# Kernel optimization log

Hardware: AMD Instinct MI355X
Metric: run time of the kernel (lower is better)

## Reference

```python
import jax, jax.numpy as jnp
import numpy as np

ALPHA = 100.0  # self.softmax_alpha


def _interp_nearest(x, size):
    # torch F.interpolate mode='nearest': src_idx = floor(dst_idx * H_in / H_out)
    H, W = x.shape[-2], x.shape[-1]
    h, w = size
    ri = (jnp.arange(h) * H) // h
    ci = (jnp.arange(w) * W) // w
    return x[:, :, ri, :][:, :, :, ci]


def _interp_bilinear_ac(x, size):
    # torch F.interpolate mode='bilinear', align_corners=True
    H, W = x.shape[-2], x.shape[-1]
    h, w = size

    def coords(n_out, n_in):
        if n_out == 1:
            return jnp.zeros((1,), jnp.float32)
        return jnp.arange(n_out, dtype=jnp.float32) * ((n_in - 1) / (n_out - 1))

    ry, rx = coords(h, H), coords(w, W)
    y0 = jnp.floor(ry).astype(jnp.int32)
    x0 = jnp.floor(rx).astype(jnp.int32)
    y1 = jnp.clip(y0 + 1, 0, H - 1)
    x1 = jnp.clip(x0 + 1, 0, W - 1)
    wy = (ry - y0.astype(jnp.float32))[None, None, :, None]
    wx = (rx - x0.astype(jnp.float32))[None, None, None, :]
    rows = x[:, :, y0, :] * (1.0 - wy) + x[:, :, y1, :] * wy  # (n,c,h,W)
    return rows[:, :, :, x0] * (1.0 - wx) + rows[:, :, :, x1] * wx  # (n,c,h,w)


def _warp(unalign_fb, fa, fa_parse, fb, fb_parse, alpha):
    n, c, h, w = fa.shape
    c2 = unalign_fb.shape[1]
    hw = h * w
    # center and channel-normalize features per spatial location
    fa = fa - jnp.mean(fa, axis=(2, 3), keepdims=True)
    fb = fb - jnp.mean(fb, axis=(2, 3), keepdims=True)
    fa = fa.reshape(n, c, hw)
    fb = fb.reshape(n, c, hw)
    fa = fa / jnp.linalg.norm(fa, axis=1, keepdims=True)
    fb = fb / jnp.linalg.norm(fb, axis=1, keepdims=True)
    ufb = unalign_fb.reshape(n, c2, hw)
    mask_a = (fa_parse.reshape(n, -1, hw)[:, 1:, :] != 0).astype(fa.dtype)  # (n,K,hw)
    mask_b = (fb_parse.reshape(n, -1, hw)[:, 1:, :] != 0).astype(fb.dtype)
    local_fa = fa[:, None, :, :] * mask_a[:, :, None, :]  # (n,K,c,hw)
    local_fb = fb[:, None, :, :] * mask_b[:, :, None, :]  # (n,K,c,hw)
    # energy[n,k,q,p] = sum_c local_fb[n,k,c,q] * local_fa[n,k,c,p]
    energy = jnp.einsum('nkcq,nkcp->nkqp', local_fb, local_fa) * alpha
    corr = jax.nn.softmax(energy, axis=2)  # softmax over fb locations q
    warped = jnp.einsum('ncq,nkqp->nkcp', ufb, corr)  # (n,K,c2,hw)
    combined = (warped * mask_a[:, :, None, :]).sum(axis=1)  # (n,c2,hw)
    norm = jnp.maximum(mask_a.sum(axis=1, keepdims=True), 1.0)  # (n,1,hw)
    aligned = combined / norm
    return aligned.reshape(n, c2, h, w)


def setup_inputs() -> dict:
    key = jax.random.key(0)
    k1, k2, k3, k4, k5 = jax.random.split(key, 5)
    return {
        'unalign_fb': jax.random.normal(k1, (1, 64, 256, 256), jnp.float32),
        'fa': jax.random.normal(k2, (1, 256, 64, 64), jnp.float32),
        'fa_parse': jax.random.randint(k3, (1, 4, 256, 256), 0, 2).astype(jnp.int32),
        'fb': jax.random.normal(k4, (1, 256, 64, 64), jnp.float32),
        'fb_parse': jax.random.randint(k5, (1, 4, 256, 256), 0, 2).astype(jnp.int32),
    }


def reference(unalign_fb, fa, fa_parse, fb, fb_parse):
    raw_hw = unalign_fb.shape[-2:]
    feat_hw = fa.shape[-2:]
    fa_p = _interp_nearest(fa_parse, feat_hw)
    fb_p = _interp_nearest(fb_parse, feat_hw)
    ufb = _interp_bilinear_ac(unalign_fb, fb.shape[-2:])
    aligned = _warp(ufb, fa, fa_p, fb, fb_p, ALPHA)
    return _interp_bilinear_ac(aligned, raw_hw)
```

## Files before the change

### kernel.cpp

```cpp
#include <hip/hip_runtime.h>
#include <math.h>

#define HW 4096
#define CC 256
#define C2 64
#define E50f 1.928749848e-22f

typedef unsigned short USH;
typedef __attribute__((ext_vector_type(8))) _Float16 f16x8;
typedef __attribute__((ext_vector_type(8))) short bf8;
typedef __attribute__((ext_vector_type(4))) float f32x4;

__device__ __forceinline__ USH f2bf(float x) {
    unsigned u = __float_as_uint(x);
    u += 0x7fff + ((u >> 16) & 1);
    return (USH)(u >> 16);
}
__device__ __forceinline__ USH f2h(float x) {
    _Float16 h = (_Float16)x;
    return *(USH*)&h;
}

__device__ __forceinline__ void gl2lds16(const USH* g, USH* l) {
    __builtin_amdgcn_global_load_lds(
        (const __attribute__((address_space(1))) void*)g,
        (__attribute__((address_space(3))) void*)l, 16, 0, 0);
}

__global__ void k_prep1(const float* __restrict__ fa, const float* __restrict__ fb,
                        float* __restrict__ mu,
                        const float* __restrict__ ufb_src, const int* __restrict__ fb_parse,
                        USH* __restrict__ vtT, float* __restrict__ bgp) {
    __shared__ float4 sred[256];
    int t = threadIdx.x;
    if (blockIdx.x < 512) {
        int b = blockIdx.x;
        const float* src = (b < CC) ? (fa + b * HW) : (fb + (b - CC) * HW);
        float s = 0.f;
        for (int q = t; q < HW; q += 256) s += src[q];
        sred[t].x = s;
        __syncthreads();
        for (int st = 128; st > 0; st >>= 1) {
            if (t < st) sred[t].x += sred[t + st].x;
            __syncthreads();
        }
        if (t == 0) mu[b] = sred[0].x * (1.0f / HW);
        return;
    }
    int bid = blockIdx.x - 512;
    int pblk = bid & 15, c = bid >> 4;
    int p = pblk * 256 + t;
    int j = p >> 6, i = p & 63;
    int off = (4 * j) * 256 + 4 * i;
    float m0 = (fb_parse[1 * 65536 + off] != 0) ? 1.f : 0.f;
    float m1 = (fb_parse[2 * 65536 + off] != 0) ? 1.f : 0.f;
    float m2 = (fb_parse[3 * 65536 + off] != 0) ? 1.f : 0.f;
    float ry = j * (255.0f / 63.0f);
    int y0 = (int)ry; y0 = min(y0, 255); int y1 = min(y0 + 1, 255);
    float wy = ry - (float)y0;
    float rx = i * (255.0f / 63.0f);
    int x0 = (int)rx; x0 = min(x0, 255); int x1 = min(x0 + 1, 255);
    float wx = rx - (float)x0;
    const float* sc = ufb_src + c * 65536;
    float r0 = sc[y0 * 256 + x0] * (1.f - wx) + sc[y0 * 256 + x1] * wx;
    float r1 = sc[y1 * 256 + x0] * (1.f - wx) + sc[y1 * 256 + x1] * wx;
    float v = r0 * (1.f - wy) + r1 * wy;
    size_t cbase = (size_t)(p >> 5) * 8192 + (p & 31);
    vtT[cbase + (0 * 65 + c) * 32] = f2bf(v * m0);
    vtT[cbase + (1 * 65 + c) * 32] = f2bf(v * m1);
    vtT[cbase + (2 * 65 + c) * 32] = f2bf(v * m2);
    if (c == 0) {
        vtT[cbase + 64 * 32]  = f2bf(m0);
        vtT[cbase + 129 * 32] = f2bf(m1);
        vtT[cbase + 194 * 32] = f2bf(m2);
        for (int m = 195; m < 256; ++m) vtT[cbase + m * 32] = 0;
    }
    sred[t] = make_float4(v, v * m0, v * m1, v * m2);
    __syncthreads();
    for (int st = 128; st > 0; st >>= 1) {
        if (t < st) {
            float4 o = sred[t + st];
            sred[t].x += o.x; sred[t].y += o.y; sred[t].z += o.z; sred[t].w += o.w;
        }
        __syncthreads();
    }
    if (t == 0) {
        float4 r = sred[0];
        bgp[pblk * 320 + 256 + c]     = r.x;
        bgp[pblk * 320 + 0 * 65 + c]  = r.y;
        bgp[pblk * 320 + 1 * 65 + c]  = r.z;
        bgp[pblk * 320 + 2 * 65 + c]  = r.w;
    }
    __syncthreads();
    if (c == 0) {
        sred[t] = make_float4(m0, m1, m2, 0.f);
        __syncthreads();
        for (int st = 128; st > 0; st >>= 1) {
            if (t < st) {
                float4 o = sred[t + st];
                sred[t].x += o.x; sred[t].y += o.y; sred[t].z += o.z;
            }
            __syncthreads();
        }
        if (t == 0) {
            float4 r = sred[0];
            bgp[pblk * 320 + 64]  = r.x;
            bgp[pblk * 320 + 129] = r.y;
            bgp[pblk * 320 + 194] = r.z;
        }
    }
}

__global__ __launch_bounds__(256) void k_normT(
    const float* __restrict__ fa, const float* __restrict__ fb,
    const float* __restrict__ mu_,
    USH* __restrict__ faT, USH* __restrict__ fbT) {
    __shared__ float tile[256][33];
    __shared__ float red[8][32];
    __shared__ float rv[32];
    int which = blockIdx.z;
    const float* src = which ? fb : fa;
    USH* dst = which ? fbT : faT;
    const float* mu = mu_ + which * CC;
    int p0 = blockIdx.x * 32;
    int t = threadIdx.x;
    int pi = t & 31, g = t >> 5;
    for (int it = 0; it < 32; ++it) {
        int c = it * 8 + g;
        tile[c][pi] = src[(size_t)c * HW + p0 + pi];
    }
    __syncthreads();
    float ss = 0.f;
#pragma unroll
    for (int jc = 0; jc < 32; ++jc) {
        float v = tile[g * 32 + jc][pi] - mu[g * 32 + jc];
        ss += v * v;
    }
    red[g][pi] = ss;
    __syncthreads();
    if (g == 0) {
        float s2 = 0.f;
#pragma unroll
        for (int gg = 0; gg < 8; ++gg) s2 += red[gg][pi];
        rv[pi] = rsqrtf(s2);
    }
    __syncthreads();
    float rinv = rv[pi];
    size_t base = (size_t)g * 131072 + (size_t)(p0 + pi) * 32;
#pragma unroll
    for (int seg = 0; seg < 4; ++seg) {
        union { USH us[8]; uint4 v; } h;
#pragma unroll
        for (int jc = 0; jc < 8; ++jc)
            h.us[jc] = f2h((tile[g * 32 + seg * 8 + jc][pi] - mu[g * 32 + seg * 8 + jc]) * rinv);
        *(uint4*)&dst[base + seg * 8] = h.v;
    }
}

__global__ __launch_bounds__(512, 2) void k_attn(
    const USH* __restrict__ faT, const USH* __restrict__ fbT,
    const USH* __restrict__ vtT, float* __restrict__ part) {
    __shared__ USH sA[8 * 4096];
    __shared__ USH sE[128 * 136];
    int t = threadIdx.x;
    int bid = blockIdx.x;
    int z = bid & 7;
    int p0 = (bid >> 3) * 128;
    int w = t >> 6, lane = t & 63, lr = lane & 15, quad = lane >> 4;
    f32x4 accp[2][8] = {};

#pragma unroll
    for (int seg = 0; seg < 8; ++seg)
        gl2lds16(faT + (size_t)w * 131072 + (size_t)p0 * 32 + seg * 512 + lane * 8,
                 &sA[w * 4096 + seg * 512]);

    const USH* pB = fbT + (size_t)(z * 512 + 16 * w + lr) * 32 + quad * 8;
    const USH* pV = vtT + (size_t)(32 * w + lr) * 32 + quad * 8;

    __syncthreads();

    for (int qt = 0; qt < 4; ++qt) {
        f32x4 accs[8] = {};
#pragma unroll
        for (int kc = 0; kc < 8; ++kc) {
            f16x8 a, b[8];
            a = *(const f16x8*)&pB[(size_t)kc * 131072 + qt * 4096];
#pragma unroll
            for (int jj = 0; jj < 8; ++jj)
                b[jj] = *(const f16x8*)&sA[kc * 4096 + (16 * jj + lr) * 32 + quad * 8];
#pragma unroll
            for (int jj = 0; jj < 8; ++jj)
                accs[jj] = __builtin_amdgcn_mfma_f32_16x16x32_f16(a, b[jj], accs[jj], 0, 0, 0);
        }
        if (qt) __syncthreads();
#pragma unroll
        for (int jj = 0; jj < 8; ++jj) {
            unsigned u0 = ((unsigned)f2bf(__expf(fmaf(100.f, accs[jj][1], -50.f))) << 16)
                        | (unsigned)f2bf(__expf(fmaf(100.f, accs[jj][0], -50.f)));
            unsigned u1 = ((unsigned)f2bf(__expf(fmaf(100.f, accs[jj][3], -50.f))) << 16)
                        | (unsigned)f2bf(__expf(fmaf(100.f, accs[jj][2], -50.f)));
            int addr = (16 * jj + lr) * 136 + 16 * w + 4 * quad;
            uint2 u; u.x = u0; u.y = u1;
            *(uint2*)&sE[addr] = u;
        }
        __syncthreads();
#pragma unroll
        for (int kc = 0; kc < 4; ++kc) {
            size_t vb = (size_t)(z * 16 + qt * 4 + kc) * 8192;
            bf8 av[2] = {}, be[8];
#pragma unroll
            for (int i = 0; i < 2; ++i)
                if (!(w == 7 || (w == 6 && i == 1)))
                    av[i] = *(const bf8*)&pV[vb + i * 512];
#pragma unroll
            for (int jj = 0; jj < 8; ++jj)
                be[jj] = *(const bf8*)&sE[(16 * jj + lr) * 136 + kc * 32 + quad * 8];
#pragma unroll
            for (int i = 0; i < 2; ++i)
#pragma unroll
                for (int jj = 0; jj < 8; ++jj)
                    if (!(w == 7 || (w == 6 && i == 1)))
                        accp[i][jj] = __builtin_amdgcn_mfma_f32_16x16x32_bf16(av[i], be[jj], accp[i][jj], 0, 0, 0);
        }
    }
    float* op = part + (size_t)z * 1048576;
#pragma unroll
    for (int i = 0; i < 2; ++i) {
        int m = 32 * w + 16 * i + 4 * quad;
#pragma unroll
        for (int jj = 0; jj < 8; ++jj) {
            int pc = p0 + 16 * jj + lr;
#pragma unroll
            for (int r = 0; r < 4; ++r)
                if (m + r < 195)
                    op[(size_t)(m + r) * HW + pc] = accp[i][jj][r];
        }
    }
}

__global__ void k_combine8(const float* __restrict__ part, const float* __restrict__ bgp,
                           const int* __restrict__ fa_parse, float* __restrict__ aligned) {
    __shared__ float sden[3];
    __shared__ float sc2[4][4];
    int t = threadIdx.x;
    int cg = blockIdx.y * 4;
    if (t < 19) {
        int idx;
        if (t < 3) idx = t * 65 + 64;
        else {
            int lc = (t - 3) >> 2, r = (t - 3) & 3;
            idx = (r < 3) ? r * 65 + (cg + lc) : 256 + (cg + lc);
        }
        float s = 0.f;
#pragma unroll
        for (int pb = 0; pb < 16; ++pb) s += bgp[pb * 320 + idx];
        if (t < 3) sden[t] = s;
        else sc2[(t - 3) >> 2][(t - 3) & 3] = s;
    }
    __syncthreads();
    int p = blockIdx.x * 256 + t;
    int jj = p >> 6, ii = p & 63;
    int off = (4 * jj) * 256 + 4 * ii;
    float ma[3], den[3];
    float s = 0.f;
#pragma unroll
    for (int k = 0; k < 3; ++k) {
        ma[k] = (fa_parse[(k + 1) * 65536 + off] != 0) ? 1.f : 0.f;
        s += ma[k];
        den[k] = E50f * (4096.0f - sden[k]);
        size_t rd = (size_t)(k * 65 + 64) * HW + p;
#pragma unroll
        for (int z = 0; z < 8; ++z) den[k] += part[(size_t)z * 1048576 + rd];
    }
    float fs = fmaxf(s, 1.f);
#pragma unroll
    for (int lc = 0; lc < 4; ++lc) {
        int c2 = cg + lc;
        float num = 0.f;
#pragma unroll
        for (int k = 0; k < 3; ++k) {
            float nu = E50f * (sc2[lc][3] - sc2[lc][k]);
            size_t rn = (size_t)(k * 65 + c2) * HW + p;
#pragma unroll
            for (int z = 0; z < 8; ++z) nu += part[(size_t)z * 1048576 + rn];
            num += ma[k] * (nu / den[k]);
        }
        aligned[(size_t)c2 * HW + p] = num / fs;
    }
}

__global__ void k_bilin_up(const float* __restrict__ aligned, float* __restrict__ out) {
    int idx = (blockIdx.x * 256 + threadIdx.x) * 4;
    int c2 = blockIdx.y;
    int y = idx >> 8;
    float ry = y * (63.0f / 255.0f);
    int y0 = (int)ry; y0 = min(y0, 63); int y1 = min(y0 + 1, 63);
    float wy = ry - (float)y0;
    const float* a = aligned + c2 * HW;
    float4 o;
    float* op = &o.x;
#pragma unroll
    for (int u = 0; u < 4; ++u) {
        int x = (idx & 255) + u;
        float rx = x * (63.0f / 255.0f);
        int x0 = (int)rx; x0 = min(x0, 63); int x1 = min(x0 + 1, 63);
        float wx = rx - (float)x0;
        float r0 = a[y0 * 64 + x0] * (1.f - wx) + a[y0 * 64 + x1] * wx;
        float r1 = a[y1 * 64 + x0] * (1.f - wx) + a[y1 * 64 + x1] * wx;
        op[u] = r0 * (1.f - wy) + r1 * wy;
    }
    *(float4*)&out[c2 * 65536 + idx] = o;
}

extern "C" void kernel_launch(void* const* d_in, const int* in_sizes, int n_in,
                              void* d_out, int out_size, void* d_ws, size_t ws_size,
                              hipStream_t stream) {
    const float* unalign_fb = (const float*)d_in[0];
    const float* fa         = (const float*)d_in[1];
    const int*   fa_parse   = (const int*)d_in[2];
    const float* fb         = (const float*)d_in[3];
    const int*   fb_parse   = (const int*)d_in[4];
    float* out = (float*)d_out;

    float* w = (float*)d_ws;
    float* mu       = w;
    float* bgp      = w + 66048;
    float* part     = w + 71168;
    float* aligned  = w + 8459776;
    USH* faT = (USH*)(w + 8721920);
    USH* fbT = (USH*)(w + 9246208);
    USH* vtT = (USH*)(w + 9770496);

    k_prep1<<<dim3(1536), dim3(256), 0, stream>>>(fa, fb, mu, unalign_fb, fb_parse, vtT, bgp);
    k_normT<<<dim3(128, 1, 2), dim3(256), 0, stream>>>(fa, fb, mu, faT, fbT);
    k_attn<<<dim3(256), dim3(512), 0, stream>>>(faT, fbT, vtT, part);
    k_combine8<<<dim3(16, 16), dim3(256), 0, stream>>>(part, bgp, fa_parse, aligned);
    k_bilin_up<<<dim3(64, 64), dim3(256), 0, stream>>>(aligned, out);
}
```

Baseline: 129.3 us.

## Software-pipeline QK^T of next tile with PV of current tile in attention kernel

Moves the first energy-tile GEMM ahead of the loop, then in each iteration computes the next q-tile's energy MFMAs interleaved with the current tile's PV MFMAs. The exponentiated tile is staged in a double-buffered LDS array, so the next tile's softmax tile can be written while the current one is still being read. The goal is to overlap global fb loads and MFMA chains across the two GEMMs so they hide each other's latency. In exchange it doubles the sE shared memory and adds live accumulator registers, which may hurt occupancy at 512 threads with 2 blocks per CU.

```diff
diff --git a/kernel.cpp b/kernel.cpp
--- a/kernel.cpp
+++ b/kernel.cpp
@@ -161,7 +161,7 @@
     const USH* __restrict__ faT, const USH* __restrict__ fbT,
     const USH* __restrict__ vtT, float* __restrict__ part) {
     __shared__ USH sA[8 * 4096];
-    __shared__ USH sE[128 * 136];
+    __shared__ USH sE[2][128 * 136];
     int t = threadIdx.x;
     int bid = blockIdx.x;
     int z = bid & 7;
@@ -179,20 +179,23 @@
 
     __syncthreads();
 
+    f32x4 accs[8] = {};
+#pragma unroll
+    for (int kc = 0; kc < 8; ++kc) {
+        f16x8 a = *(const f16x8*)&pB[(size_t)kc * 131072];
+        f16x8 b[8];
+#pragma unroll
+        for (int jj = 0; jj < 8; ++jj)
+            b[jj] = *(const f16x8*)&sA[kc * 4096 + (16 * jj + lr) * 32 + quad * 8];
+#pragma unroll
+        for (int jj = 0; jj < 8; ++jj)
+            accs[jj] = __builtin_amdgcn_mfma_f32_16x16x32_f16(a, b[jj], accs[jj], 0, 0, 0);
+    }
+
+    int cur = 0;
     for (int qt = 0; qt < 4; ++qt) {
-        f32x4 accs[8] = {};
-#pragma unroll
-        for (int kc = 0; kc < 8; ++kc) {
-            f16x8 a, b[8];
-            a = *(const f16x8*)&pB[(size_t)kc * 131072 + qt * 4096];
-#pragma unroll
-            for (int jj = 0; jj < 8; ++jj)
-                b[jj] = *(const f16x8*)&sA[kc * 4096 + (16 * jj + lr) * 32 + quad * 8];
-#pragma unroll
-            for (int jj = 0; jj < 8; ++jj)
-                accs[jj] = __builtin_amdgcn_mfma_f32_16x16x32_f16(a, b[jj], accs[jj], 0, 0, 0);
-        }
         if (qt) __syncthreads();
+        USH* sEc = &sE[cur][0];
 #pragma unroll
         for (int jj = 0; jj < 8; ++jj) {
             unsigned u0 = ((unsigned)f2bf(__expf(fmaf(100.f, accs[jj][1], -50.f))) << 16)
@@ -201,27 +204,76 @@
                         | (unsigned)f2bf(__expf(fmaf(100.f, accs[jj][2], -50.f)));
             int addr = (16 * jj + lr) * 136 + 16 * w + 4 * quad;
             uint2 u; u.x = u0; u.y = u1;
-            *(uint2*)&sE[addr] = u;
+            *(uint2*)&sEc[addr] = u;
         }
         __syncthreads();
-#pragma unroll
-        for (int kc = 0; kc < 4; ++kc) {
-            size_t vb = (size_t)(z * 16 + qt * 4 + kc) * 8192;
-            bf8 av[2] = {}, be[8];
-#pragma unroll
-            for (int i = 0; i < 2; ++i)
-                if (!(w == 7 || (w == 6 && i == 1)))
-                    av[i] = *(const bf8*)&pV[vb + i * 512];
-#pragma unroll
-            for (int jj = 0; jj < 8; ++jj)
-                be[jj] = *(const bf8*)&sE[(16 * jj + lr) * 136 + kc * 32 + quad * 8];
-#pragma unroll
-            for (int i = 0; i < 2; ++i)
+        f32x4 nacc[8] = {};
+        if (qt < 3) {
+#pragma unroll
+            for (int u = 0; u < 4; ++u) {
+                {
+                    int kc = 2 * u;
+                    f16x8 a = *(const f16x8*)&pB[(size_t)kc * 131072 + (qt + 1) * 4096];
+                    f16x8 b[8];
+#pragma unroll
+                    for (int jj = 0; jj < 8; ++jj)
+                        b[jj] = *(const f16x8*)&sA[kc * 4096 + (16 * jj + lr) * 32 + quad * 8];
+#pragma unroll
+                    for (int jj = 0; jj < 8; ++jj)
+                        nacc[jj] = __builtin_amdgcn_mfma_f32_16x16x32_f16(a, b[jj], nacc[jj], 0, 0, 0);
+                }
+                {
+                    size_t vb = (size_t)(z * 16 + qt * 4 + u) * 8192;
+                    bf8 av[2] = {}, be[8];
+#pragma unroll
+                    for (int i = 0; i < 2; ++i)
+                        if (!(w == 7 || (w == 6 && i == 1)))
+                            av[i] = *(const bf8*)&pV[vb + i * 512];
+#pragma unroll
+                    for (int jj = 0; jj < 8; ++jj)
+                        be[jj] = *(const bf8*)&sEc[(16 * jj + lr) * 136 + u * 32 + quad * 8];
+#pragma unroll
+                    for (int i = 0; i < 2; ++i)
+#pragma unroll
+                        for (int jj = 0; jj < 8; ++jj)
+                            if (!(w == 7 || (w == 6 && i == 1)))
+                                accp[i][jj] = __builtin_amdgcn_mfma_f32_16x16x32_bf16(av[i], be[jj], accp[i][jj], 0, 0, 0);
+                }
+                {
+                    int kc = 2 * u + 1;
+                    f16x8 a = *(const f16x8*)&pB[(size_t)kc * 131072 + (qt + 1) * 4096];
+                    f16x8 b[8];
+#pragma unroll
+                    for (int jj = 0; jj < 8; ++jj)
+                        b[jj] = *(const f16x8*)&sA[kc * 4096 + (16 * jj + lr) * 32 + quad * 8];
+#pragma unroll
+                    for (int jj = 0; jj < 8; ++jj)
+                        nacc[jj] = __builtin_amdgcn_mfma_f32_16x16x32_f16(a, b[jj], nacc[jj], 0, 0, 0);
+                }
+            }
+        } else {
+#pragma unroll
+            for (int kc = 0; kc < 4; ++kc) {
+                size_t vb = (size_t)(z * 16 + qt * 4 + kc) * 8192;
+                bf8 av[2] = {}, be[8];
+#pragma unroll
+                for (int i = 0; i < 2; ++i)
+                    if (!(w == 7 || (w == 6 && i == 1)))
+                        av[i] = *(const bf8*)&pV[vb + i * 512];
 #pragma unroll
                 for (int jj = 0; jj < 8; ++jj)
-                    if (!(w == 7 || (w == 6 && i == 1)))
-                        accp[i][jj] = __builtin_amdgcn_mfma_f32_16x16x32_bf16(av[i], be[jj], accp[i][jj], 0, 0, 0);
-        }
+                    be[jj] = *(const bf8*)&sEc[(16 * jj + lr) * 136 + kc * 32 + quad * 8];
+#pragma unroll
+                for (int i = 0; i < 2; ++i)
+#pragma unroll
+                    for (int jj = 0; jj < 8; ++jj)
+                        if (!(w == 7 || (w == 6 && i == 1)))
+                            accp[i][jj] = __builtin_amdgcn_mfma_f32_16x16x32_bf16(av[i], be[jj], accp[i][jj], 0, 0, 0);
+            }
+        }
+#pragma unroll
+        for (int jj = 0; jj < 8; ++jj) accs[jj] = nacc[jj];
+        cur ^= 1;
     }
     float* op = part + (size_t)z * 1048576;
 #pragma unroll
```

New measurement: 130.9 us. About the same (+1.2%).

## Fuse partial combine with bilinear upsample through shared-memory row bands

Applied to the files above, without the earlier changes.

Merges the combine kernel and the bilinear upsampling kernel into one: each block computes the aligned rows needed for a 64-row output band of one channel into LDS, then upsamples directly to the output. This removes a kernel launch and the global write/read of the intermediate aligned tensor. In exchange, the denominator partial sums and parse masks are recomputed per channel instead of shared across four channels, and overlapping row bands are recomputed, increasing reads of the partial buffer.

```diff
diff --git a/kernel.cpp b/kernel.cpp
--- a/kernel.cpp
+++ b/kernel.cpp
@@ -238,78 +238,78 @@
     }
 }
 
-__global__ void k_combine8(const float* __restrict__ part, const float* __restrict__ bgp,
-                           const int* __restrict__ fa_parse, float* __restrict__ aligned) {
+__global__ __launch_bounds__(256) void k_final(
+    const float* __restrict__ part, const float* __restrict__ bgp,
+    const int* __restrict__ fa_parse, float* __restrict__ out) {
+    __shared__ float sal[18 * 64];
     __shared__ float sden[3];
-    __shared__ float sc2[4][4];
+    __shared__ float sc2v[4];
     int t = threadIdx.x;
-    int cg = blockIdx.y * 4;
-    if (t < 19) {
-        int idx;
-        if (t < 3) idx = t * 65 + 64;
-        else {
-            int lc = (t - 3) >> 2, r = (t - 3) & 3;
-            idx = (r < 3) ? r * 65 + (cg + lc) : 256 + (cg + lc);
-        }
+    int c2 = blockIdx.y;
+    int q = blockIdx.x;
+    if (t < 7) {
+        int idx = (t < 3) ? (t * 65 + 64) : ((t < 6) ? (t - 3) * 65 + c2 : 256 + c2);
         float s = 0.f;
 #pragma unroll
         for (int pb = 0; pb < 16; ++pb) s += bgp[pb * 320 + idx];
-        if (t < 3) sden[t] = s;
-        else sc2[(t - 3) >> 2][(t - 3) & 3] = s;
-    }
-    __syncthreads();
-    int p = blockIdx.x * 256 + t;
-    int jj = p >> 6, ii = p & 63;
-    int off = (4 * jj) * 256 + 4 * ii;
-    float ma[3], den[3];
-    float s = 0.f;
-#pragma unroll
-    for (int k = 0; k < 3; ++k) {
-        ma[k] = (fa_parse[(k + 1) * 65536 + off] != 0) ? 1.f : 0.f;
-        s += ma[k];
-        den[k] = E50f * (4096.0f - sden[k]);
-        size_t rd = (size_t)(k * 65 + 64) * HW + p;
-#pragma unroll
-        for (int z = 0; z < 8; ++z) den[k] += part[(size_t)z * 1048576 + rd];
-    }
-    float fs = fmaxf(s, 1.f);
-#pragma unroll
-    for (int lc = 0; lc < 4; ++lc) {
-        int c2 = cg + lc;
-        float num = 0.f;
-#pragma unroll
-        for (int k = 0; k < 3; ++k) {
-            float nu = E50f * (sc2[lc][3] - sc2[lc][k]);
-            size_t rn = (size_t)(k * 65 + c2) * HW + p;
-#pragma unroll
-            for (int z = 0; z < 8; ++z) nu += part[(size_t)z * 1048576 + rn];
-            num += ma[k] * (nu / den[k]);
-        }
-        aligned[(size_t)c2 * HW + p] = num / fs;
-    }
-}
-
-__global__ void k_bilin_up(const float* __restrict__ aligned, float* __restrict__ out) {
-    int idx = (blockIdx.x * 256 + threadIdx.x) * 4;
-    int c2 = blockIdx.y;
-    int y = idx >> 8;
-    float ry = y * (63.0f / 255.0f);
-    int y0 = (int)ry; y0 = min(y0, 63); int y1 = min(y0 + 1, 63);
-    float wy = ry - (float)y0;
-    const float* a = aligned + c2 * HW;
-    float4 o;
-    float* op = &o.x;
-#pragma unroll
-    for (int u = 0; u < 4; ++u) {
-        int x = (idx & 255) + u;
-        float rx = x * (63.0f / 255.0f);
-        int x0 = (int)rx; x0 = min(x0, 63); int x1 = min(x0 + 1, 63);
-        float wx = rx - (float)x0;
-        float r0 = a[y0 * 64 + x0] * (1.f - wx) + a[y0 * 64 + x1] * wx;
-        float r1 = a[y1 * 64 + x0] * (1.f - wx) + a[y1 * 64 + x1] * wx;
-        op[u] = r0 * (1.f - wy) + r1 * wy;
-    }
-    *(float4*)&out[c2 * 65536 + idx] = o;
+        if (t < 3) sden[t] = s; else sc2v[t - 3] = s;
+    }
+    __syncthreads();
+    int a0 = (64 * q * 63) / 255;
+    int nrows = min(18, 64 - a0);
+    int nval = nrows * 64;
+    for (int it = 0; it < 5; ++it) {
+        int idx = it * 256 + t;
+        if (idx < nval) {
+            int p = (a0 + (idx >> 6)) * 64 + (idx & 63);
+            int off = (4 * (p >> 6)) * 256 + 4 * (p & 63);
+            float ma[3], den[3];
+            float s = 0.f;
+#pragma unroll
+            for (int k = 0; k < 3; ++k) {
+                ma[k] = (fa_parse[(k + 1) * 65536 + off] != 0) ? 1.f : 0.f;
+                s += ma[k];
+                den[k] = E50f * (4096.0f - sden[k]);
+                size_t rd = (size_t)(k * 65 + 64) * HW + p;
+#pragma unroll
+                for (int z = 0; z < 8; ++z) den[k] += part[(size_t)z * 1048576 + rd];
+            }
+            float num = 0.f;
+#pragma unroll
+            for (int k = 0; k < 3; ++k) {
+                float nu = E50f * (sc2v[3] - sc2v[k]);
+                size_t rn = (size_t)(k * 65 + c2) * HW + p;
+#pragma unroll
+                for (int z = 0; z < 8; ++z) nu += part[(size_t)z * 1048576 + rn];
+                num += ma[k] * (nu / den[k]);
+            }
+            sal[idx] = num / fmaxf(s, 1.f);
+        }
+    }
+    __syncthreads();
+    float* op = out + (size_t)c2 * 65536 + (size_t)q * 64 * 256;
+    for (int it = 0; it < 16; ++it) {
+        int lin = (it * 256 + t) * 4;
+        int y = 64 * q + (lin >> 8);
+        float ry = y * (63.0f / 255.0f);
+        int y0 = (int)ry; y0 = min(y0, 63); int y1 = min(y0 + 1, 63);
+        float wy = ry - (float)y0;
+        const float* r0p = &sal[(y0 - a0) * 64];
+        const float* r1p = &sal[(y1 - a0) * 64];
+        float4 o;
+        float* ov = &o.x;
+#pragma unroll
+        for (int u = 0; u < 4; ++u) {
+            int x = (lin & 255) + u;
+            float rx = x * (63.0f / 255.0f);
+            int x0 = (int)rx; x0 = min(x0, 63); int x1 = min(x0 + 1, 63);
+            float wx = rx - (float)x0;
+            float r0 = r0p[x0] * (1.f - wx) + r0p[x1] * wx;
+            float r1 = r1p[x0] * (1.f - wx) + r1p[x1] * wx;
+            ov[u] = r0 * (1.f - wy) + r1 * wy;
+        }
+        *(float4*)&op[lin] = o;
+    }
 }
 
 extern "C" void kernel_launch(void* const* d_in, const int* in_sizes, int n_in,
@@ -326,7 +326,6 @@
     float* mu       = w;
     float* bgp      = w + 66048;
     float* part     = w + 71168;
-    float* aligned  = w + 8459776;
     USH* faT = (USH*)(w + 8721920);
     USH* fbT = (USH*)(w + 9246208);
     USH* vtT = (USH*)(w + 9770496);
@@ -334,6 +333,5 @@
     k_prep1<<<dim3(1536), dim3(256), 0, stream>>>(fa, fb, mu, unalign_fb, fb_parse, vtT, bgp);
     k_normT<<<dim3(128, 1, 2), dim3(256), 0, stream>>>(fa, fb, mu, faT, fbT);
     k_attn<<<dim3(256), dim3(512), 0, stream>>>(faT, fbT, vtT, part);
-    k_combine8<<<dim3(16, 16), dim3(256), 0, stream>>>(part, bgp, fa_parse, aligned);
-    k_bilin_up<<<dim3(64, 64), dim3(256), 0, stream>>>(aligned, out);
-}
+    k_final<<<dim3(4, 64), dim3(256), 0, stream>>>(part, bgp, fa_parse, out);
+}
```

New measurement: 131.4 us. Within noise of the previous version (+1.6%).
